# Performance work log

Measured on AMD Instinct MI355X. Metric: run time of the kernel, lower is better.

The kernel has to match this reference:

```python
import jax, jax.numpy as jnp
import numpy as np

B, T, H, S = 2, 2048, 16, 64
EMB = H * S  # 1024


def layer_norm(x, g, b, eps=1e-5):
    mu = jnp.mean(x, axis=-1, keepdims=True)
    var = jnp.var(x, axis=-1, keepdims=True)
    return (x - mu) * jax.lax.rsqrt(var + eps) * g + b


def setup_inputs() -> dict:
    key = jax.random.key(0)
    ks = jax.random.split(key, 12)
    sc = 0.02
    return {
        "x": jax.random.normal(ks[0], (B, T, EMB), dtype=jnp.float32),
        "Wkqv": jax.random.normal(ks[1], (S, 3 * S), dtype=jnp.float32) * sc,
        "Wproj": jax.random.normal(ks[2], (EMB, EMB), dtype=jnp.float32) * sc,
        "g1": jnp.ones((EMB,), jnp.float32),
        "b1": jnp.zeros((EMB,), jnp.float32),
        "W1": jax.random.normal(ks[3], (EMB, 4 * EMB), dtype=jnp.float32) * sc,
        "bff1": jnp.zeros((4 * EMB,), jnp.float32),
        "W2": jax.random.normal(ks[4], (4 * EMB, EMB), dtype=jnp.float32) * sc,
        "bff2": jnp.zeros((EMB,), jnp.float32),
        "g2": jnp.ones((EMB,), jnp.float32),
        "b2": jnp.zeros((EMB,), jnp.float32),
    }


def reference(x, Wkqv, Wproj, g1, b1, W1, bff1, W2, bff2, g2, b2):
    Bb, Tt, _ = x.shape
    xh = x.reshape(Bb, Tt, H, S)                     # [B,T,H,S]
    kqv = jnp.einsum('bths,sd->bthd', xh, Wkqv)      # [B,T,H,3S], shared per-head weight
    k, q, v = jnp.split(kqv, 3, axis=-1)             # note order: k, q, v
    scores = jnp.einsum('bihk,bjhk->bijh', q, k) / jnp.sqrt(jnp.float32(S))
    att = jax.nn.softmax(scores, axis=2)             # softmax over key dim j
    res = jnp.einsum('btih,bihs->bths', att, v).reshape(Bb, Tt, EMB)
    mha = res @ Wproj                                # Linear(emb, emb, bias=False)
    x = layer_norm(x + mha, g1, b1)
    h = jax.nn.gelu(x @ W1 + bff1, approximate=False)
    ff = h @ W2 + bff2
    return layer_norm(x + ff, g2, b2)
```

## Files before the change

kernel.cpp:

```cpp
#include <hip/hip_runtime.h>
#include <hip/hip_bf16.h>
#include <math.h>

#define B_ 2
#define T_ 2048
#define H_ 16
#define S_ 64
#define EMB 1024
#define FF 4096
#define BT (B_*T_)
#define ROWS (B_*T_*H_)

typedef __attribute__((ext_vector_type(8))) short s16x8;
typedef __attribute__((ext_vector_type(4))) float f32x4;

struct P4 { unsigned short* p[4]; };

__device__ __forceinline__ unsigned short f2b(float f) {
    return __builtin_bit_cast(unsigned short, __float2bfloat16(f));
}
__device__ __forceinline__ float b2f(short u) {
    return __builtin_bit_cast(float, ((unsigned int)(unsigned short)u) << 16);
}

__device__ __forceinline__ void gl_lds16(const void* g, void* l) {
    __builtin_amdgcn_global_load_lds(
        (const __attribute__((address_space(1))) void*)g,
        (__attribute__((address_space(3))) void*)l, 16, 0, 0);
}

__device__ __forceinline__ f32x4 mfma16(s16x8 a, s16x8 b, f32x4 c) {
    return __builtin_amdgcn_mfma_f32_16x16x32_bf16(a, b, c, 0, 0, 0);
}

__global__ __launch_bounds__(256) void kqv_kernel(const float* __restrict__ x,
        const unsigned short* __restrict__ Wqt, unsigned short* __restrict__ K,
        unsigned short* __restrict__ Q, unsigned short* __restrict__ V) {
    const int tid = threadIdx.x;
    const int w = tid >> 6, lane = tid & 63;
    const int l15 = lane & 15, quad = lane >> 4;
    const long r0 = (long)blockIdx.x * 128 + w * 32;

    s16x8 af[2][2];
    #pragma unroll
    for (int mt = 0; mt < 2; ++mt)
        #pragma unroll
        for (int ks = 0; ks < 2; ++ks) {
            const float* xp = x + (r0 + mt*16 + l15) * 64 + ks*32 + quad*8;
            const float4 v0 = *(const float4*)xp;
            const float4 v1 = *(const float4*)(xp + 4);
            s16x8 a;
            a[0] = (short)f2b(v0.x); a[1] = (short)f2b(v0.y);
            a[2] = (short)f2b(v0.z); a[3] = (short)f2b(v0.w);
            a[4] = (short)f2b(v1.x); a[5] = (short)f2b(v1.y);
            a[6] = (short)f2b(v1.z); a[7] = (short)f2b(v1.w);
            af[mt][ks] = a;
        }

    #pragma unroll
    for (int nt = 0; nt < 12; ++nt) {
        const s16x8 b0 = *(const s16x8*)&Wqt[(nt*16 + l15)*64 + quad*8];
        const s16x8 b1 = *(const s16x8*)&Wqt[(nt*16 + l15)*64 + 32 + quad*8];
        f32x4 acc[2] = {};
        #pragma unroll
        for (int mt = 0; mt < 2; ++mt) {
            acc[mt] = mfma16(af[mt][0], b0, acc[mt]);
            acc[mt] = mfma16(af[mt][1], b1, acc[mt]);
        }
        unsigned short* dst = (nt < 4) ? K : (nt < 8) ? Q : V;
        const int c0 = (nt & 3) * 16 + l15;
        #pragma unroll
        for (int mt = 0; mt < 2; ++mt)
            #pragma unroll
            for (int r = 0; r < 4; ++r)
                dst[(r0 + mt*16 + quad*4 + r) * 64 + c0] = f2b(acc[mt][r]);
    }
}

__global__ __launch_bounds__(256) void attn_kernel(const unsigned short* __restrict__ Q,
        const unsigned short* __restrict__ K, const unsigned short* __restrict__ V,
        unsigned short* __restrict__ res) {
    __shared__ __align__(16) unsigned short Ks[64 * 64];
    __shared__ __align__(16) unsigned short Vt[64 * 64];
    __shared__ __align__(16) unsigned short Ps[4][32 * 72];
    const int tid = threadIdx.x;
    const int w = tid >> 6, lane = tid & 63;
    const int l15 = lane & 15, quad = lane >> 4;
    const int qt = blockIdx.x;
    const int bh = blockIdx.y;
    const int b = bh >> 4, h = bh & 15;
    const long base = ((long)b * (T_ * H_) + h) * 64;
    const unsigned short* Qp = Q + base;
    const unsigned short* Kp = K + base;
    const unsigned short* Vp = V + base;
    const int q0 = qt * 128;

    s16x8 qf[2][2];
    #pragma unroll
    for (int mt = 0; mt < 2; ++mt)
        #pragma unroll
        for (int ks = 0; ks < 2; ++ks) {
            const s16x8 raw = *(const s16x8*)&Qp[(long)(q0 + w*32 + mt*16 + l15) * 1024 + ks*32 + quad*8];
            s16x8 q;
            #pragma unroll
            for (int j = 0; j < 8; ++j) q[j] = (short)f2b(b2f(raw[j]) * 0.125f);
            qf[mt][ks] = q;
        }

    s16x8 onef;
    #pragma unroll
    for (int j = 0; j < 8; ++j) onef[j] = (short)0x3F80;

    f32x4 oacc[2][4] = {};
    f32x4 lacc[2] = {};

    const int sjp = tid & 31, sd0 = (tid >> 5) * 8;
    for (int kt = 0; kt < T_ / 64; ++kt) {
        __syncthreads();
        #pragma unroll
        for (int i = 0; i < 2; ++i) {
            const int id = i * 256 + tid;
            const int j = id >> 3, dc = id & 7;
            const s16x8 kv = *(const s16x8*)&Kp[(long)(kt*64 + j) * 1024 + dc*8];
            *(s16x8*)&Ks[j*64 + ((dc ^ (j & 7)) * 8)] = kv;
        }
        {
            const int j0 = sjp * 2;
            const s16x8 va = *(const s16x8*)&Vp[(long)(kt*64 + j0)     * 1024 + sd0];
            const s16x8 vb = *(const s16x8*)&Vp[(long)(kt*64 + j0 + 1) * 1024 + sd0];
            const int jc = j0 >> 3;
            #pragma unroll
            for (int ii = 0; ii < 8; ++ii) {
                const unsigned int pk = (unsigned int)(unsigned short)va[ii]
                                      | ((unsigned int)(unsigned short)vb[ii] << 16);
                const int d = sd0 + ii;
                *(unsigned int*)&Vt[d*64 + ((jc ^ (d & 7)) * 8) + (j0 & 7)] = pk;
            }
        }
        __syncthreads();

        f32x4 s[2][4] = {};
        #pragma unroll
        for (int ks = 0; ks < 2; ++ks)
            #pragma unroll
            for (int nt = 0; nt < 4; ++nt) {
                const int j = nt*16 + l15;
                const s16x8 kf = *(const s16x8*)&Ks[j*64 + (((ks*4 + quad) ^ (l15 & 7)) * 8)];
                s[0][nt] = mfma16(qf[0][ks], kf, s[0][nt]);
                s[1][nt] = mfma16(qf[1][ks], kf, s[1][nt]);
            }

        #pragma unroll
        for (int mt = 0; mt < 2; ++mt)
            #pragma unroll
            for (int r = 0; r < 4; ++r)
                #pragma unroll
                for (int nt = 0; nt < 4; ++nt)
                    Ps[w][(mt*16 + quad*4 + r)*72 + nt*16 + l15] =
                        f2b(__expf(s[mt][nt][r]));

        #pragma unroll
        for (int ks2 = 0; ks2 < 2; ++ks2) {
            s16x8 pf[2];
            pf[0] = *(const s16x8*)&Ps[w][(l15)*72      + ks2*32 + quad*8];
            pf[1] = *(const s16x8*)&Ps[w][(16 + l15)*72 + ks2*32 + quad*8];
            lacc[0] = mfma16(pf[0], onef, lacc[0]);
            lacc[1] = mfma16(pf[1], onef, lacc[1]);
            #pragma unroll
            for (int nt = 0; nt < 4; ++nt) {
                const int d = nt*16 + l15;
                const s16x8 vf = *(const s16x8*)&Vt[d*64 + (((ks2*4 + quad) ^ (d & 7)) * 8)];
                oacc[0][nt] = mfma16(pf[0], vf, oacc[0][nt]);
                oacc[1][nt] = mfma16(pf[1], vf, oacc[1][nt]);
            }
        }
    }

    #pragma unroll
    for (int mt = 0; mt < 2; ++mt) {
        #pragma unroll
        for (int r = 0; r < 4; ++r) {
            const float inv = 1.f / lacc[mt][r];
            const int t = q0 + w*32 + mt*16 + quad*4 + r;
            #pragma unroll
            for (int nt = 0; nt < 4; ++nt)
                res[((long)(b * T_ + t)) * EMB + h*64 + nt*16 + l15] =
                    f2b(oacc[mt][nt][r] * inv);
        }
    }
}

__global__ __launch_bounds__(256) void gemm_gelu(const unsigned short* __restrict__ A,
        const unsigned short* __restrict__ Bt, const float* __restrict__ bias,
        unsigned short* __restrict__ C, int M, int N, int Kd) {
    __shared__ __align__(16) unsigned short As[128 * 32];
    __shared__ __align__(16) unsigned short Bs[128 * 32];
    const int tid = threadIdx.x;
    const int w = tid >> 6, lane = tid & 63;
    const int l15 = lane & 15, quad = lane >> 4;
    const int wm = w >> 1, wn = w & 1;
    const int bn = blockIdx.x, bm = blockIdx.y;
    const int sr = lane >> 2, skq = lane & 3;
    f32x4 acc[4][4] = {};
    const long arow = (long)(bm*128 + w*32 + sr);
    const long brow = (long)(bn*128 + w*32 + sr);

    for (int kt = 0; kt < Kd; kt += 32) {
        gl_lds16(A  + (arow     )*Kd + kt + skq*8, (char*)As + (w*32     )*64 + lane*16);
        gl_lds16(A  + (arow + 16)*Kd + kt + skq*8, (char*)As + (w*32 + 16)*64 + lane*16);
        gl_lds16(Bt + (brow     )*Kd + kt + skq*8, (char*)Bs + (w*32     )*64 + lane*16);
        gl_lds16(Bt + (brow + 16)*Kd + kt + skq*8, (char*)Bs + (w*32 + 16)*64 + lane*16);
        __syncthreads();
        s16x8 af[4], bf[4];
        #pragma unroll
        for (int mt = 0; mt < 4; ++mt)
            af[mt] = *(const s16x8*)&As[(wm*64 + mt*16 + l15)*32 + quad*8];
        #pragma unroll
        for (int nt = 0; nt < 4; ++nt)
            bf[nt] = *(const s16x8*)&Bs[(wn*64 + nt*16 + l15)*32 + quad*8];
        #pragma unroll
        for (int mt = 0; mt < 4; ++mt)
            #pragma unroll
            for (int nt = 0; nt < 4; ++nt)
                acc[mt][nt] = mfma16(af[mt], bf[nt], acc[mt][nt]);
        __syncthreads();
    }

    #pragma unroll
    for (int mt = 0; mt < 4; ++mt) {
        const int row0 = bm*128 + wm*64 + mt*16 + quad*4;
        #pragma unroll
        for (int nt = 0; nt < 4; ++nt) {
            const int col = bn*128 + wn*64 + nt*16 + l15;
            const float bv = bias[col];
            #pragma unroll
            for (int r = 0; r < 4; ++r) {
                float v = acc[mt][nt][r] + bv;
                v = 0.5f * v * (1.f + erff(v * 0.70710678118654752440f));
                C[(long)(row0 + r)*N + col] = f2b(v);
            }
        }
    }
}

__global__ __launch_bounds__(256) void gemm_splitk(const unsigned short* __restrict__ A,
        const unsigned short* __restrict__ Bt, P4 parts, int M, int N, int Kd, int Ks) {
    __shared__ __align__(16) unsigned short As[128 * 32];
    __shared__ __align__(16) unsigned short Bs[128 * 32];
    const int tid = threadIdx.x;
    const int w = tid >> 6, lane = tid & 63;
    const int l15 = lane & 15, quad = lane >> 4;
    const int wm = w >> 1, wn = w & 1;
    const int bn = blockIdx.x, bm = blockIdx.y, s = blockIdx.z;
    const int sr = lane >> 2, skq = lane & 3;
    f32x4 acc[4][4] = {};
    const long arow = (long)(bm*128 + w*32 + sr);
    const long brow = (long)(bn*128 + w*32 + sr);
    const int k0 = s * Ks;

    for (int kt = k0; kt < k0 + Ks; kt += 32) {
        gl_lds16(A  + (arow     )*Kd + kt + skq*8, (char*)As + (w*32     )*64 + lane*16);
        gl_lds16(A  + (arow + 16)*Kd + kt + skq*8, (char*)As + (w*32 + 16)*64 + lane*16);
        gl_lds16(Bt + (brow     )*Kd + kt + skq*8, (char*)Bs + (w*32     )*64 + lane*16);
        gl_lds16(Bt + (brow + 16)*Kd + kt + skq*8, (char*)Bs + (w*32 + 16)*64 + lane*16);
        __syncthreads();
        s16x8 af[4], bf[4];
        #pragma unroll
        for (int mt = 0; mt < 4; ++mt)
            af[mt] = *(const s16x8*)&As[(wm*64 + mt*16 + l15)*32 + quad*8];
        #pragma unroll
        for (int nt = 0; nt < 4; ++nt)
            bf[nt] = *(const s16x8*)&Bs[(wn*64 + nt*16 + l15)*32 + quad*8];
        #pragma unroll
        for (int mt = 0; mt < 4; ++mt)
            #pragma unroll
            for (int nt = 0; nt < 4; ++nt)
                acc[mt][nt] = mfma16(af[mt], bf[nt], acc[mt][nt]);
        __syncthreads();
    }

    unsigned short* Cp = parts.p[s];
    #pragma unroll
    for (int mt = 0; mt < 4; ++mt) {
        const int row0 = bm*128 + wm*64 + mt*16 + quad*4;
        #pragma unroll
        for (int nt = 0; nt < 4; ++nt) {
            const int col = bn*128 + wn*64 + nt*16 + l15;
            #pragma unroll
            for (int r = 0; r < 4; ++r)
                Cp[(long)(row0 + r)*N + col] = f2b(acc[mt][nt][r]);
        }
    }
}

template <int P>
__global__ __launch_bounds__(256) void ln_kernel(const float* __restrict__ xa,
        P4 parts, const float* __restrict__ addb, const float* __restrict__ g,
        const float* __restrict__ bia, float* __restrict__ out,
        unsigned short* __restrict__ outb) {
    const int row = blockIdx.x;
    const int tid = threadIdx.x;
    float4 v = ((const float4*)(xa + (long)row * EMB))[tid];
    #pragma unroll
    for (int p = 0; p < P; ++p) {
        const ushort4 u = ((const ushort4*)(parts.p[p] + (long)row * EMB))[tid];
        v.x += b2f((short)u.x); v.y += b2f((short)u.y);
        v.z += b2f((short)u.z); v.w += b2f((short)u.w);
    }
    if (addb) {
        const float4 ab = ((const float4*)addb)[tid];
        v.x += ab.x; v.y += ab.y; v.z += ab.z; v.w += ab.w;
    }
    float s = v.x + v.y + v.z + v.w;
    float ss = v.x * v.x + v.y * v.y + v.z * v.z + v.w * v.w;
    #pragma unroll
    for (int off = 32; off > 0; off >>= 1) {
        s += __shfl_down(s, off, 64);
        ss += __shfl_down(ss, off, 64);
    }
    __shared__ float ls[4], lss[4];
    __shared__ float mean_s, rstd_s;
    const int wid = tid >> 6, lane = tid & 63;
    if (lane == 0) { ls[wid] = s; lss[wid] = ss; }
    __syncthreads();
    if (tid == 0) {
        const float S0 = ls[0] + ls[1] + ls[2] + ls[3];
        const float S2 = lss[0] + lss[1] + lss[2] + lss[3];
        const float mean = S0 * (1.f / EMB);
        const float var = S2 * (1.f / EMB) - mean * mean;
        mean_s = mean;
        rstd_s = rsqrtf(var + 1e-5f);
    }
    __syncthreads();
    const float mean = mean_s, rstd = rstd_s;
    const float4 gg = ((const float4*)g)[tid];
    const float4 bb = ((const float4*)bia)[tid];
    float4 o;
    o.x = (v.x - mean) * rstd * gg.x + bb.x;
    o.y = (v.y - mean) * rstd * gg.y + bb.y;
    o.z = (v.z - mean) * rstd * gg.z + bb.z;
    o.w = (v.w - mean) * rstd * gg.w + bb.w;
    ((float4*)(out + (long)row * EMB))[tid] = o;
    if (outb) {
        unsigned short* ob = outb + (long)row * EMB + tid * 4;
        ob[0] = f2b(o.x); ob[1] = f2b(o.y); ob[2] = f2b(o.z); ob[3] = f2b(o.w);
    }
}

__global__ __launch_bounds__(256) void transp_all(const float* __restrict__ Wp,
        const float* __restrict__ W1, const float* __restrict__ W2,
        const float* __restrict__ Wq, unsigned short* __restrict__ Wpt,
        unsigned short* __restrict__ W1t, unsigned short* __restrict__ W2t,
        unsigned short* __restrict__ Wqt) {
    int id = blockIdx.x;
    const float* W; unsigned short* Wt; int Kd, N, ntx;
    if (id < 1024)      {            W = Wp; Wt = Wpt; Kd = 1024; N = 1024; ntx = 32; }
    else if (id < 5120) { id -= 1024; W = W1; Wt = W1t; Kd = 1024; N = 4096; ntx = 128; }
    else if (id < 9216) { id -= 5120; W = W2; Wt = W2t; Kd = 4096; N = 1024; ntx = 32; }
    else                { id -= 9216; W = Wq; Wt = Wqt; Kd = 64;   N = 192;  ntx = 6;  }
    __shared__ float Ts[32][33];
    const int tid = threadIdx.x;
    const int n0 = (id % ntx) * 32, k0 = (id / ntx) * 32;
    const int r = tid >> 3, c4 = (tid & 7) * 4;
    const float4 v = *(const float4*)&W[(long)(k0 + r) * N + n0 + c4];
    Ts[r][c4] = v.x; Ts[r][c4 + 1] = v.y; Ts[r][c4 + 2] = v.z; Ts[r][c4 + 3] = v.w;
    __syncthreads();
    #pragma unroll
    for (int i = 0; i < 4; ++i)
        Wt[(long)(n0 + r) * Kd + k0 + c4 + i] = f2b(Ts[c4 + i][r]);
}

extern "C" void kernel_launch(void* const* d_in, const int* in_sizes, int n_in,
                              void* d_out, int out_size, void* d_ws, size_t ws_size,
                              hipStream_t stream) {
    (void)in_sizes; (void)n_in; (void)out_size;
    const float* x     = (const float*)d_in[0];
    const float* Wkqv  = (const float*)d_in[1];
    const float* Wproj = (const float*)d_in[2];
    const float* g1    = (const float*)d_in[3];
    const float* b1    = (const float*)d_in[4];
    const float* W1    = (const float*)d_in[5];
    const float* bff1  = (const float*)d_in[6];
    const float* W2    = (const float*)d_in[7];
    const float* bff2  = (const float*)d_in[8];
    const float* g2    = (const float*)d_in[9];
    const float* b2    = (const float*)d_in[10];
    float* out = (float*)d_out;
    char* ws = (char*)d_ws;

    const size_t MB = 1u << 20;
    unsigned short* Qb   = (unsigned short*)(ws + 0 * MB);
    unsigned short* Kb   = (unsigned short*)(ws + 8 * MB);
    unsigned short* Vb   = (unsigned short*)(ws + 16 * MB);
    unsigned short* resb = (unsigned short*)(ws + 24 * MB);
    unsigned short* hb   = (unsigned short*)(ws + 8 * MB);
    unsigned short* mp0  = (unsigned short*)(ws + 40 * MB);
    unsigned short* mp1  = (unsigned short*)(ws + 48 * MB);
    float*          x1   = (float*)(ws + 56 * MB);
    unsigned short* x1b  = Qb;
    unsigned short* Wpt  = (unsigned short*)(ws + 72 * MB);
    unsigned short* W1t  = (unsigned short*)(ws + 74 * MB);
    unsigned short* W2t  = (unsigned short*)(ws + 82 * MB);
    unsigned short* Wqt  = (unsigned short*)(ws + 90 * MB);
    unsigned short* fp2  = (unsigned short*)(ws + 91 * MB);
    unsigned short* fp3  = (unsigned short*)(ws + 99 * MB);
    const bool big = ws_size >= 108 * MB;

    transp_all<<<dim3(9228), 256, 0, stream>>>(Wproj, W1, W2, Wkqv, Wpt, W1t, W2t, Wqt);

    kqv_kernel<<<dim3(ROWS/128), 256, 0, stream>>>(x, Wqt, Kb, Qb, Vb);
    attn_kernel<<<dim3(T_/128, B_*H_), 256, 0, stream>>>(Qb, Kb, Vb, resb);
    P4 mp; mp.p[0] = mp0; mp.p[1] = mp1; mp.p[2] = nullptr; mp.p[3] = nullptr;
    gemm_splitk<<<dim3(EMB/128, BT/128, 2), 256, 0, stream>>>(resb, Wpt, mp, BT, EMB, EMB, EMB/2);
    ln_kernel<2><<<dim3(BT), 256, 0, stream>>>(x, mp, nullptr, g1, b1, x1, x1b);
    gemm_gelu<<<dim3(FF/128, BT/128), 256, 0, stream>>>(x1b, W1t, bff1, hb, BT, FF, EMB);
    if (big) {
        P4 fp; fp.p[0] = mp0; fp.p[1] = mp1; fp.p[2] = fp2; fp.p[3] = fp3;
        gemm_splitk<<<dim3(EMB/128, BT/128, 4), 256, 0, stream>>>(hb, W2t, fp, BT, EMB, FF, FF/4);
        ln_kernel<4><<<dim3(BT), 256, 0, stream>>>(x1, fp, bff2, g2, b2, out, nullptr);
    } else {
        P4 fp; fp.p[0] = mp0; fp.p[1] = mp1; fp.p[2] = nullptr; fp.p[3] = nullptr;
        gemm_splitk<<<dim3(EMB/128, BT/128, 2), 256, 0, stream>>>(hb, W2t, fp, BT, EMB, FF, FF/2);
        ln_kernel<2><<<dim3(BT), 256, 0, stream>>>(x1, fp, bff2, g2, b2, out, nullptr);
    }
}
```

Baseline: 372.1 us.

## Split attention over key halves with combine kernel; drop fp32 residual copy

The attention kernel now splits the key range into two halves along a new grid dimension (split-KV). Each half writes unnormalized bf16 partial outputs and row sums, and a new combine kernel adds and normalizes them. This doubles the number of attention blocks for better occupancy across CUs, at the cost of extra partial-buffer traffic and an extra launch. The score MFMA is transposed so the exp'd probabilities are stored as packed 8-byte LDS writes. The first layernorm no longer writes an fp32 x1, and the second layernorm reads the bf16 x1b residual instead, which adds rounding error to the residual.

```diff
diff --git a/kernel.cpp b/kernel.cpp
--- a/kernel.cpp
+++ b/kernel.cpp
@@ -79,7 +79,7 @@
 
 __global__ __launch_bounds__(256) void attn_kernel(const unsigned short* __restrict__ Q,
         const unsigned short* __restrict__ K, const unsigned short* __restrict__ V,
-        unsigned short* __restrict__ res) {
+        unsigned short* __restrict__ Po, float* __restrict__ Pl) {
     __shared__ __align__(16) unsigned short Ks[64 * 64];
     __shared__ __align__(16) unsigned short Vt[64 * 64];
     __shared__ __align__(16) unsigned short Ps[4][32 * 72];
@@ -88,6 +88,7 @@
     const int l15 = lane & 15, quad = lane >> 4;
     const int qt = blockIdx.x;
     const int bh = blockIdx.y;
+    const int sidx = blockIdx.z;
     const int b = bh >> 4, h = bh & 15;
     const long base = ((long)b * (T_ * H_) + h) * 64;
     const unsigned short* Qp = Q + base;
@@ -115,7 +116,8 @@
     f32x4 lacc[2] = {};
 
     const int sjp = tid & 31, sd0 = (tid >> 5) * 8;
-    for (int kt = 0; kt < T_ / 64; ++kt) {
+    const int kt0 = sidx * 16;
+    for (int kt = kt0; kt < kt0 + 16; ++kt) {
         __syncthreads();
         #pragma unroll
         for (int i = 0; i < 2; ++i) {
@@ -139,25 +141,30 @@
         }
         __syncthreads();
 
-        f32x4 s[2][4] = {};
+        f32x4 sT[4][2] = {};
         #pragma unroll
         for (int ks = 0; ks < 2; ++ks)
             #pragma unroll
-            for (int nt = 0; nt < 4; ++nt) {
-                const int j = nt*16 + l15;
+            for (int jt = 0; jt < 4; ++jt) {
+                const int j = jt*16 + l15;
                 const s16x8 kf = *(const s16x8*)&Ks[j*64 + (((ks*4 + quad) ^ (l15 & 7)) * 8)];
-                s[0][nt] = mfma16(qf[0][ks], kf, s[0][nt]);
-                s[1][nt] = mfma16(qf[1][ks], kf, s[1][nt]);
+                sT[jt][0] = mfma16(kf, qf[0][ks], sT[jt][0]);
+                sT[jt][1] = mfma16(kf, qf[1][ks], sT[jt][1]);
             }
 
         #pragma unroll
-        for (int mt = 0; mt < 2; ++mt)
-            #pragma unroll
-            for (int r = 0; r < 4; ++r)
-                #pragma unroll
-                for (int nt = 0; nt < 4; ++nt)
-                    Ps[w][(mt*16 + quad*4 + r)*72 + nt*16 + l15] =
-                        f2b(__expf(s[mt][nt][r]));
+        for (int jt = 0; jt < 4; ++jt)
+            #pragma unroll
+            for (int qt2 = 0; qt2 < 2; ++qt2) {
+                const float e0 = __expf(sT[jt][qt2][0]);
+                const float e1 = __expf(sT[jt][qt2][1]);
+                const float e2 = __expf(sT[jt][qt2][2]);
+                const float e3 = __expf(sT[jt][qt2][3]);
+                uint2 pk;
+                pk.x = (unsigned int)f2b(e0) | ((unsigned int)f2b(e1) << 16);
+                pk.y = (unsigned int)f2b(e2) | ((unsigned int)f2b(e3) << 16);
+                *(uint2*)&Ps[w][(qt2*16 + l15)*72 + jt*16 + quad*4] = pk;
+            }
 
         #pragma unroll
         for (int ks2 = 0; ks2 < 2; ++ks2) {
@@ -176,18 +183,35 @@
         }
     }
 
+    const long po_row = (long)(sidx * 32 + bh) * T_;
     #pragma unroll
     for (int mt = 0; mt < 2; ++mt) {
         #pragma unroll
         for (int r = 0; r < 4; ++r) {
-            const float inv = 1.f / lacc[mt][r];
             const int t = q0 + w*32 + mt*16 + quad*4 + r;
+            if (l15 == 0) Pl[po_row + t] = lacc[mt][r];
             #pragma unroll
             for (int nt = 0; nt < 4; ++nt)
-                res[((long)(b * T_ + t)) * EMB + h*64 + nt*16 + l15] =
-                    f2b(oacc[mt][nt][r] * inv);
-        }
-    }
+                Po[(po_row + t)*64 + nt*16 + l15] = f2b(oacc[mt][nt][r]);
+        }
+    }
+}
+
+__global__ __launch_bounds__(256) void attn_combine(const unsigned short* __restrict__ Po,
+        const float* __restrict__ Pl, unsigned short* __restrict__ res) {
+    const int idx = blockIdx.x * 256 + threadIdx.x;
+    const int d4 = idx & 15, bht = idx >> 4;
+    const ushort4 a = ((const ushort4*)Po)[(long)bht * 16 + d4];
+    const ushort4 c = ((const ushort4*)Po)[((long)bht + 32L*T_) * 16 + d4];
+    const float inv = 1.f / (Pl[bht] + Pl[bht + 32*T_]);
+    const int bh = bht >> 11, t = bht & (T_ - 1);
+    const int b = bh >> 4, h = bh & 15;
+    uint2 o;
+    o.x = (unsigned int)f2b((b2f((short)a.x) + b2f((short)c.x)) * inv)
+        | ((unsigned int)f2b((b2f((short)a.y) + b2f((short)c.y)) * inv) << 16);
+    o.y = (unsigned int)f2b((b2f((short)a.z) + b2f((short)c.z)) * inv)
+        | ((unsigned int)f2b((b2f((short)a.w) + b2f((short)c.w)) * inv) << 16);
+    *(uint2*)&res[(long)(b * T_ + t) * EMB + h*64 + d4*4] = o;
 }
 
 __global__ __launch_bounds__(256) void gemm_gelu(const unsigned short* __restrict__ A,
@@ -293,14 +317,21 @@
     }
 }
 
-template <int P>
-__global__ __launch_bounds__(256) void ln_kernel(const float* __restrict__ xa,
+template <int P, int XBF>
+__global__ __launch_bounds__(256) void ln_kernel(const void* __restrict__ xa,
         P4 parts, const float* __restrict__ addb, const float* __restrict__ g,
         const float* __restrict__ bia, float* __restrict__ out,
         unsigned short* __restrict__ outb) {
     const int row = blockIdx.x;
     const int tid = threadIdx.x;
-    float4 v = ((const float4*)(xa + (long)row * EMB))[tid];
+    float4 v;
+    if (XBF) {
+        const ushort4 u = ((const ushort4*)xa)[(long)row * (EMB/4) + tid];
+        v.x = b2f((short)u.x); v.y = b2f((short)u.y);
+        v.z = b2f((short)u.z); v.w = b2f((short)u.w);
+    } else {
+        v = ((const float4*)xa)[(long)row * (EMB/4) + tid];
+    }
     #pragma unroll
     for (int p = 0; p < P; ++p) {
         const ushort4 u = ((const ushort4*)(parts.p[p] + (long)row * EMB))[tid];
@@ -340,7 +371,7 @@
     o.y = (v.y - mean) * rstd * gg.y + bb.y;
     o.z = (v.z - mean) * rstd * gg.z + bb.z;
     o.w = (v.w - mean) * rstd * gg.w + bb.w;
-    ((float4*)(out + (long)row * EMB))[tid] = o;
+    if (out) ((float4*)(out + (long)row * EMB))[tid] = o;
     if (outb) {
         unsigned short* ob = outb + (long)row * EMB + tid * 4;
         ob[0] = f2b(o.x); ob[1] = f2b(o.y); ob[2] = f2b(o.z); ob[3] = f2b(o.w);
@@ -394,9 +425,10 @@
     unsigned short* Vb   = (unsigned short*)(ws + 16 * MB);
     unsigned short* resb = (unsigned short*)(ws + 24 * MB);
     unsigned short* hb   = (unsigned short*)(ws + 8 * MB);
+    unsigned short* Po   = (unsigned short*)(ws + 40 * MB);
+    float*          Pl   = (float*)(ws + 56 * MB);
     unsigned short* mp0  = (unsigned short*)(ws + 40 * MB);
     unsigned short* mp1  = (unsigned short*)(ws + 48 * MB);
-    float*          x1   = (float*)(ws + 56 * MB);
     unsigned short* x1b  = Qb;
     unsigned short* Wpt  = (unsigned short*)(ws + 72 * MB);
     unsigned short* W1t  = (unsigned short*)(ws + 74 * MB);
@@ -409,18 +441,19 @@
     transp_all<<<dim3(9228), 256, 0, stream>>>(Wproj, W1, W2, Wkqv, Wpt, W1t, W2t, Wqt);
 
     kqv_kernel<<<dim3(ROWS/128), 256, 0, stream>>>(x, Wqt, Kb, Qb, Vb);
-    attn_kernel<<<dim3(T_/128, B_*H_), 256, 0, stream>>>(Qb, Kb, Vb, resb);
+    attn_kernel<<<dim3(T_/128, B_*H_, 2), 256, 0, stream>>>(Qb, Kb, Vb, Po, Pl);
+    attn_combine<<<dim3(32*T_*16/256), 256, 0, stream>>>(Po, Pl, resb);
     P4 mp; mp.p[0] = mp0; mp.p[1] = mp1; mp.p[2] = nullptr; mp.p[3] = nullptr;
     gemm_splitk<<<dim3(EMB/128, BT/128, 2), 256, 0, stream>>>(resb, Wpt, mp, BT, EMB, EMB, EMB/2);
-    ln_kernel<2><<<dim3(BT), 256, 0, stream>>>(x, mp, nullptr, g1, b1, x1, x1b);
+    ln_kernel<2, 0><<<dim3(BT), 256, 0, stream>>>(x, mp, nullptr, g1, b1, nullptr, x1b);
     gemm_gelu<<<dim3(FF/128, BT/128), 256, 0, stream>>>(x1b, W1t, bff1, hb, BT, FF, EMB);
     if (big) {
         P4 fp; fp.p[0] = mp0; fp.p[1] = mp1; fp.p[2] = fp2; fp.p[3] = fp3;
         gemm_splitk<<<dim3(EMB/128, BT/128, 4), 256, 0, stream>>>(hb, W2t, fp, BT, EMB, FF, FF/4);
-        ln_kernel<4><<<dim3(BT), 256, 0, stream>>>(x1, fp, bff2, g2, b2, out, nullptr);
+        ln_kernel<4, 1><<<dim3(BT), 256, 0, stream>>>(x1b, fp, bff2, g2, b2, out, nullptr);
     } else {
         P4 fp; fp.p[0] = mp0; fp.p[1] = mp1; fp.p[2] = nullptr; fp.p[3] = nullptr;
         gemm_splitk<<<dim3(EMB/128, BT/128, 2), 256, 0, stream>>>(hb, W2t, fp, BT, EMB, FF, FF/2);
-        ln_kernel<2><<<dim3(BT), 256, 0, stream>>>(x1, fp, bff2, g2, b2, out, nullptr);
-    }
-}
+        ln_kernel<2, 1><<<dim3(BT), 256, 0, stream>>>(x1b, fp, bff2, g2, b2, out, nullptr);
+    }
+}
```

Result: no change. 374.3 us (+0.6%).
